# Optimization experiments

Hardware: AMD Instinct MI355X
Metric: run time of the kernel (lower is better)

## Reference

```python
import jax, jax.numpy as jnp
import numpy as np
import itertools

GRID = 256          # voxel grid extent per axis (coords in [0, GRID))
KSIZE = 3           # kernel_size
OFFSETS = np.array(list(itertools.product(range(KSIZE), repeat=3)), dtype=np.int32) - (KSIZE // 2)  # [27,3]


def setup_inputs() -> dict:
    key = jax.random.key(0)
    k1, k2, k3 = jax.random.split(key, 3)
    N, Cin, Cout = 262144, 64, 64
    coords = jax.random.randint(k1, (N, 3), 0, GRID, dtype=jnp.int32)
    feats = jax.random.normal(k2, (N, Cin), dtype=jnp.float32)
    kernel = jax.random.normal(k3, (KSIZE ** 3, Cin, Cout), dtype=jnp.float32) * 0.02
    return {"coords": coords, "feats": feats, "kernel": kernel}


def reference(coords, feats, kernel):
    # Submanifold sparse conv3d: out[i] = sum_k feats[j_k(i)] @ kernel[k]
    # where coords[j_k(i)] == coords[i] + offset_k (if such a point exists).
    N = coords.shape[0]
    Cout = kernel.shape[-1]
    # Hash table: linearized voxel -> point index (-1 if empty).
    lin = (coords[:, 0] * GRID + coords[:, 1]) * GRID + coords[:, 2]
    table = jnp.full((GRID ** 3,), -1, dtype=jnp.int32).at[lin].set(
        jnp.arange(N, dtype=jnp.int32))
    out = jnp.zeros((N, Cout), dtype=feats.dtype)
    for k in range(KSIZE ** 3):
        off = jnp.asarray(OFFSETS[k])              # [3]
        nc = coords + off[None, :]                 # neighbor coords [N,3]
        in_bounds = jnp.all((nc >= 0) & (nc < GRID), axis=1)
        nlin = (nc[:, 0] * GRID + nc[:, 1]) * GRID + nc[:, 2]
        idx = table[jnp.clip(nlin, 0, GRID ** 3 - 1)]
        valid = in_bounds & (idx >= 0)
        g = feats[jnp.where(valid, idx, 0)] * valid[:, None].astype(feats.dtype)  # [N,Cin]
        out = out + g @ kernel[k]                  # [N,Cout]
    return out
```

## Files before the change

### kernel.cpp

```cpp
#include <hip/hip_runtime.h>

#define VGRID 256
#define N_TAPS 27
#define CIN 64
#define COUT 64
#define BPTS 128

typedef short short8 __attribute__((ext_vector_type(8)));
typedef float float4v __attribute__((ext_vector_type(4)));

__device__ __forceinline__ short f2bf(float x) {
    unsigned u = __builtin_bit_cast(unsigned, x);
    unsigned r = (u + 0x7FFF + ((u >> 16) & 1)) >> 16;
    return (short)r;
}

__global__ void __launch_bounds__(256) build_kernel(
        const int* __restrict__ coords, int* __restrict__ table,
        unsigned* __restrict__ bits, const float* __restrict__ W,
        short* __restrict__ Wt, const float* __restrict__ F,
        short* __restrict__ Fb, int n, int bt_blocks, int fb_elems) {
    int b = (int)blockIdx.x;
    if (b >= bt_blocks + N_TAPS) {
        int idx = (b - bt_blocks - N_TAPS) * 256 + (int)threadIdx.x;
        int e = idx * 8;
        if (e < fb_elems) {
            const float4v* s = (const float4v*)(F + e);
            float4v x = __builtin_nontemporal_load(s);
            float4v y = __builtin_nontemporal_load(s + 1);
            short8 o = {f2bf(x[0]), f2bf(x[1]), f2bf(x[2]), f2bf(x[3]),
                        f2bf(y[0]), f2bf(y[1]), f2bf(y[2]), f2bf(y[3])};
            *(short8*)(Fb + e) = o;
        }
        return;
    }
    if (b >= bt_blocks) {
        int tap = b - bt_blocks;
        for (int e = threadIdx.x; e < CIN * COUT; e += 256) {
            int ci = e >> 6, co = e & 63;
            int ks = ci >> 5, quad = (ci >> 3) & 3, el = ci & 7;
            Wt[((((size_t)tap * 2 + ks) * 4 + quad) * 64 + co) * 8 + el] =
                f2bf(W[((size_t)tap * CIN + ci) * COUT + co]);
        }
        return;
    }
    int i = b * 256 + threadIdx.x;
    if (i >= n) return;
    int lin = (coords[i * 3 + 0] * VGRID + coords[i * 3 + 1]) * VGRID + coords[i * 3 + 2];
    atomicMax(&table[lin], i);
    atomicOr(&bits[lin >> 5], 1u << (lin & 31));
}

template<bool BF>
__global__ void __launch_bounds__(256) fused_kernel_t(
        const int* __restrict__ coords, const int* __restrict__ table,
        const unsigned* __restrict__ bits, const float* __restrict__ feats,
        const short* __restrict__ featsb, const short* __restrict__ Wt,
        float* __restrict__ out, int n) {
    __shared__ int s_pk[BPTS];
    __shared__ unsigned s_hm[2][BPTS];
    __shared__ int s_jc[BPTS];
    __shared__ int s_p[4][BPTS];

    int t = threadIdx.x;
    int p = t & (BPTS - 1);
    int h = t >> 7;
    int i = blockIdx.x * BPTS + p;

    int cx = 0, cy = 0, cz = 0;
    unsigned pmask = 0;
    if (i < n) {
        cx = coords[i * 3 + 0];
        cy = coords[i * 3 + 1];
        cz = coords[i * 3 + 2];
        if (h == 0) s_jc[p] = table[(cx * VGRID + cy) * VGRID + cz];

        int zlo = cz > 0 ? cz - 1 : 0;
        int zhi = cz < VGRID - 1 ? cz + 1 : VGRID - 1;
        int wlo = zlo >> 5, whi = zhi >> 5;
        unsigned rwa[5], rwb[5];
#pragma unroll
        for (int rr = 0; rr < 5; ++rr) {
            int r = h * 5 + rr;
            int nx = cx + r / 3 - 1, ny = cy + r % 3 - 1;
            bool v = (r < 9) && ((unsigned)nx < VGRID) && ((unsigned)ny < VGRID);
            int rb = ((nx * VGRID + ny) * VGRID) >> 5;
            rwa[rr] = v ? bits[rb + wlo] : 0u;
            rwb[rr] = v ? bits[rb + whi] : 0u;
        }
#pragma unroll
        for (int rr = 0; rr < 5; ++rr) {
            int r = h * 5 + rr;
#pragma unroll
            for (int zz = 0; zz < 3; ++zz) {
                int k = r * 3 + zz;
                int nz = cz + zz - 1;
                if (r < 9 && k != 13 && (unsigned)nz < VGRID) {
                    unsigned wrd = ((nz >> 5) == wlo) ? rwa[rr] : rwb[rr];
                    pmask |= ((wrd >> (nz & 31)) & 1u) << k;
                }
            }
        }
    }
    if (h == 0) {
        s_pk[p] = (cx << 16) | (cy << 8) | cz;
        if (i >= n) s_jc[p] = 0;
    }
    s_hm[h][p] = pmask;
    __syncthreads();

    {
        unsigned hmc = s_hm[0][p] | s_hm[1][p];
        if (h == 0) s_hm[0][p] = hmc;
        unsigned mm = hmc;
        if (h) { mm &= mm - 1u; if (mm) mm &= mm - 1u; }
        int kA = -1, kB = -1;
        if (mm) { kA = __builtin_ctz(mm); mm &= mm - 1u;
                  if (mm) kB = __builtin_ctz(mm); }
        int ja = 0, jb = 0;
        if (kA >= 0)
            ja = table[((cx + kA / 9 - 1) * VGRID + (cy + (kA / 3) % 3 - 1)) * VGRID
                       + (cz + kA % 3 - 1)];
        if (kB >= 0)
            jb = table[((cx + kB / 9 - 1) * VGRID + (cy + (kB / 3) % 3 - 1)) * VGRID
                       + (cz + kB % 3 - 1)];
        s_p[2 * h + 0][p] = ja;
        s_p[2 * h + 1][p] = jb;
    }
    __syncthreads();

    int wave = t >> 6, lane = t & 63;
    int m = lane & 15, quad = lane >> 4;
    const short8* Bp = (const short8*)Wt;
    const short8* Fp = (const short8*)featsb;
    int base = blockIdx.x * BPTS;

    for (int gg = 0; gg < 2; ++gg) {
        int g = wave * 2 + gg;
        int row = g * 16 + m;
        unsigned rhm = s_hm[0][row];

        unsigned gor = rhm;
        gor |= (unsigned)__shfl_xor((int)gor, 1);
        gor |= (unsigned)__shfl_xor((int)gor, 2);
        gor |= (unsigned)__shfl_xor((int)gor, 4);
        gor |= (unsigned)__shfl_xor((int)gor, 8);
        gor = __builtin_amdgcn_readfirstlane(gor);

        float4v acc[4] = {{0,0,0,0},{0,0,0,0},{0,0,0,0},{0,0,0,0}};

        {
            int rjc = s_jc[row];
            short8 a0, a1;
            if constexpr (BF) {
                a0 = Fp[(size_t)rjc * 8 + quad];
                a1 = Fp[(size_t)rjc * 8 + 4 + quad];
            } else {
                const float* fr = feats + (size_t)rjc * CIN + quad * 8;
                float4v u0 = *(const float4v*)(fr);
                float4v u1 = *(const float4v*)(fr + 4);
                float4v v0 = *(const float4v*)(fr + 32);
                float4v v1 = *(const float4v*)(fr + 36);
                a0 = (short8){f2bf(u0[0]), f2bf(u0[1]), f2bf(u0[2]), f2bf(u0[3]),
                              f2bf(u1[0]), f2bf(u1[1]), f2bf(u1[2]), f2bf(u1[3])};
                a1 = (short8){f2bf(v0[0]), f2bf(v0[1]), f2bf(v0[2]), f2bf(v0[3]),
                              f2bf(v1[0]), f2bf(v1[1]), f2bf(v1[2]), f2bf(v1[3])};
            }
#pragma unroll
            for (int nt = 0; nt < 4; ++nt) {
                short8 b0 = Bp[((13 * 2 + 0) * 4 + quad) * 64 + nt * 16 + m];
                short8 b1 = Bp[((13 * 2 + 1) * 4 + quad) * 64 + nt * 16 + m];
                acc[nt] = __builtin_amdgcn_mfma_f32_16x16x32_bf16(a0, b0, acc[nt], 0, 0, 0);
                acc[nt] = __builtin_amdgcn_mfma_f32_16x16x32_bf16(a1, b1, acc[nt], 0, 0, 0);
            }
        }

        unsigned gm = gor;
        while (gm) {
            int k = (int)__builtin_ctz(gm); gm &= gm - 1u;
            bool has = (rhm >> k) & 1u;
            short8 h0 = {0,0,0,0,0,0,0,0}, h1 = {0,0,0,0,0,0,0,0};
            if (has) {
                int rank = __builtin_popcount(rhm & ((1u << k) - 1u));
                int j2;
                if (rank < 4) {
                    j2 = s_p[rank][row];
                } else {
                    int rpk = s_pk[row];
                    int rx = (rpk >> 16) & 255, ry = (rpk >> 8) & 255, rz = rpk & 255;
                    j2 = table[((rx + k / 9 - 1) * VGRID + (ry + (k / 3) % 3 - 1)) * VGRID
                               + (rz + k % 3 - 1)];
                }
                if constexpr (BF) {
                    h0 = Fp[(size_t)j2 * 8 + quad];
                    h1 = Fp[(size_t)j2 * 8 + 4 + quad];
                } else {
                    const float* hr = feats + (size_t)j2 * CIN + quad * 8;
                    float4v u0 = *(const float4v*)(hr);
                    float4v u1 = *(const float4v*)(hr + 4);
                    float4v v0 = *(const float4v*)(hr + 32);
                    float4v v1 = *(const float4v*)(hr + 36);
                    h0 = (short8){f2bf(u0[0]), f2bf(u0[1]), f2bf(u0[2]), f2bf(u0[3]),
                                  f2bf(u1[0]), f2bf(u1[1]), f2bf(u1[2]), f2bf(u1[3])};
                    h1 = (short8){f2bf(v0[0]), f2bf(v0[1]), f2bf(v0[2]), f2bf(v0[3]),
                                  f2bf(v1[0]), f2bf(v1[1]), f2bf(v1[2]), f2bf(v1[3])};
                }
            }
#pragma unroll
            for (int nt = 0; nt < 4; ++nt) {
                short8 b0 = Bp[((k * 2 + 0) * 4 + quad) * 64 + nt * 16 + m];
                short8 b1 = Bp[((k * 2 + 1) * 4 + quad) * 64 + nt * 16 + m];
                acc[nt] = __builtin_amdgcn_mfma_f32_16x16x32_bf16(h0, b0, acc[nt], 0, 0, 0);
                acc[nt] = __builtin_amdgcn_mfma_f32_16x16x32_bf16(h1, b1, acc[nt], 0, 0, 0);
            }
        }

#pragma unroll
        for (int nt = 0; nt < 4; ++nt)
#pragma unroll
            for (int r2 = 0; r2 < 4; ++r2) {
                int orow = base + g * 16 + quad * 4 + r2;
                if (orow < n)
                    __builtin_nontemporal_store(
                        acc[nt][r2], &out[(size_t)orow * COUT + nt * 16 + m]);
            }
    }
}

extern "C" void kernel_launch(void* const* d_in, const int* in_sizes, int n_in,
                              void* d_out, int out_size, void* d_ws, size_t ws_size,
                              hipStream_t stream) {
    const int* coords = (const int*)d_in[0];
    const float* feats = (const float*)d_in[1];
    const float* weights = (const float*)d_in[2];
    float* out = (float*)d_out;

    int n = in_sizes[0] / 3;

    char* ws = (char*)d_ws;
    size_t BITMAP_BYTES = (size_t)VGRID * VGRID * VGRID / 8;
    bool bf = ws_size >= ((size_t)100 << 20);
    unsigned* bits = (unsigned*)ws;
    short* wbft = (short*)(ws + BITMAP_BYTES);
    short* fb = bf ? (short*)(ws + ((size_t)4 << 20)) : nullptr;
    int* table = (int*)(ws + (bf ? ((size_t)36 << 20) : ((size_t)4 << 20)));

    hipMemsetAsync(ws, 0, BITMAP_BYTES, stream);

    int bt_blocks = (n + 255) / 256;
    int fb_elems = bf ? n * CIN : 0;
    int conv_blocks = bf ? (fb_elems / 8 + 255) / 256 : 0;
    build_kernel<<<bt_blocks + N_TAPS + conv_blocks, 256, 0, stream>>>(
        coords, table, bits, weights, wbft, feats, fb, n, bt_blocks, fb_elems);

    int f_blocks = (n + BPTS - 1) / BPTS;
    if (bf)
        fused_kernel_t<true><<<f_blocks, 256, 0, stream>>>(
            coords, table, bits, feats, fb, wbft, out, n);
    else
        fused_kernel_t<false><<<f_blocks, 256, 0, stream>>>(
            coords, table, bits, feats, fb, wbft, out, n);
}
```

Before: 209.5 us.

## Replace dense voxel table with compact open-addressing hash and pair tap processing

Swaps the 64 MB dense voxel-to-index table for a 1M-slot linear-probing hash of packed (key, index) 64-bit entries, built with atomicCAS and atomicMax. All lookups in the fused kernel go through this hash. The tap loop now handles two taps per iteration, with the center tap folded in, so more feature loads are in flight at once. The float fallback path is removed and the workspace is assumed large enough for the bf16 feature copy. This cuts table footprint and cache misses, at the cost of probe chains and an extra 8 MB memset.

```diff
diff --git a/kernel.cpp b/kernel.cpp
--- a/kernel.cpp
+++ b/kernel.cpp
@@ -5,6 +5,9 @@
 #define CIN 64
 #define COUT 64
 #define BPTS 128
+#define HBITS 20
+#define HSIZE (1u << HBITS)
+#define HEMPTY 0xFFFFFFFFFFFFFFFFull
 
 typedef short short8 __attribute__((ext_vector_type(8)));
 typedef float float4v __attribute__((ext_vector_type(4)));
@@ -15,8 +18,22 @@
     return (short)r;
 }
 
+__device__ __forceinline__ unsigned hslot(int lin) {
+    return ((unsigned)lin * 2654435761u) >> (32 - HBITS);
+}
+
+__device__ __forceinline__ int hlookup(const unsigned long long* __restrict__ hash,
+                                       int lin) {
+    unsigned s = hslot(lin);
+    for (;;) {
+        unsigned long long e = hash[s];
+        if ((unsigned)(e >> 32) == (unsigned)lin) return (int)(unsigned)e;
+        s = (s + 1) & (HSIZE - 1);
+    }
+}
+
 __global__ void __launch_bounds__(256) build_kernel(
-        const int* __restrict__ coords, int* __restrict__ table,
+        const int* __restrict__ coords, unsigned long long* __restrict__ hash,
         unsigned* __restrict__ bits, const float* __restrict__ W,
         short* __restrict__ Wt, const float* __restrict__ F,
         short* __restrict__ Fb, int n, int bt_blocks, int fb_elems) {
@@ -47,16 +64,21 @@
     int i = b * 256 + threadIdx.x;
     if (i >= n) return;
     int lin = (coords[i * 3 + 0] * VGRID + coords[i * 3 + 1]) * VGRID + coords[i * 3 + 2];
-    atomicMax(&table[lin], i);
+    unsigned long long want = ((unsigned long long)(unsigned)lin << 32) | (unsigned)i;
+    unsigned s = hslot(lin);
+    for (;;) {
+        unsigned long long old = atomicCAS(&hash[s], HEMPTY, want);
+        if (old == HEMPTY) break;
+        if ((unsigned)(old >> 32) == (unsigned)lin) { atomicMax(&hash[s], want); break; }
+        s = (s + 1) & (HSIZE - 1);
+    }
     atomicOr(&bits[lin >> 5], 1u << (lin & 31));
 }
 
-template<bool BF>
-__global__ void __launch_bounds__(256) fused_kernel_t(
-        const int* __restrict__ coords, const int* __restrict__ table,
-        const unsigned* __restrict__ bits, const float* __restrict__ feats,
-        const short* __restrict__ featsb, const short* __restrict__ Wt,
-        float* __restrict__ out, int n) {
+__global__ void __launch_bounds__(256) fused_kernel(
+        const int* __restrict__ coords, const unsigned long long* __restrict__ hash,
+        const unsigned* __restrict__ bits, const short* __restrict__ featsb,
+        const short* __restrict__ Wt, float* __restrict__ out, int n) {
     __shared__ int s_pk[BPTS];
     __shared__ unsigned s_hm[2][BPTS];
     __shared__ int s_jc[BPTS];
@@ -73,7 +95,7 @@
         cx = coords[i * 3 + 0];
         cy = coords[i * 3 + 1];
         cz = coords[i * 3 + 2];
-        if (h == 0) s_jc[p] = table[(cx * VGRID + cy) * VGRID + cz];
+        if (h == 0) s_jc[p] = hlookup(hash, (cx * VGRID + cy) * VGRID + cz);
 
         int zlo = cz > 0 ? cz - 1 : 0;
         int zhi = cz < VGRID - 1 ? cz + 1 : VGRID - 1;
@@ -119,11 +141,11 @@
                   if (mm) kB = __builtin_ctz(mm); }
         int ja = 0, jb = 0;
         if (kA >= 0)
-            ja = table[((cx + kA / 9 - 1) * VGRID + (cy + (kA / 3) % 3 - 1)) * VGRID
-                       + (cz + kA % 3 - 1)];
+            ja = hlookup(hash, ((cx + kA / 9 - 1) * VGRID + (cy + (kA / 3) % 3 - 1)) * VGRID
+                               + (cz + kA % 3 - 1));
         if (kB >= 0)
-            jb = table[((cx + kB / 9 - 1) * VGRID + (cy + (kB / 3) % 3 - 1)) * VGRID
-                       + (cz + kB % 3 - 1)];
+            jb = hlookup(hash, ((cx + kB / 9 - 1) * VGRID + (cy + (kB / 3) % 3 - 1)) * VGRID
+                               + (cz + kB % 3 - 1));
         s_p[2 * h + 0][p] = ja;
         s_p[2 * h + 1][p] = jb;
     }
@@ -139,6 +161,7 @@
         int g = wave * 2 + gg;
         int row = g * 16 + m;
         unsigned rhm = s_hm[0][row];
+        int rjc = s_jc[row];
 
         unsigned gor = rhm;
         gor |= (unsigned)__shfl_xor((int)gor, 1);
@@ -149,69 +172,54 @@
 
         float4v acc[4] = {{0,0,0,0},{0,0,0,0},{0,0,0,0},{0,0,0,0}};
 
-        {
-            int rjc = s_jc[row];
-            short8 a0, a1;
-            if constexpr (BF) {
-                a0 = Fp[(size_t)rjc * 8 + quad];
-                a1 = Fp[(size_t)rjc * 8 + 4 + quad];
-            } else {
-                const float* fr = feats + (size_t)rjc * CIN + quad * 8;
-                float4v u0 = *(const float4v*)(fr);
-                float4v u1 = *(const float4v*)(fr + 4);
-                float4v v0 = *(const float4v*)(fr + 32);
-                float4v v1 = *(const float4v*)(fr + 36);
-                a0 = (short8){f2bf(u0[0]), f2bf(u0[1]), f2bf(u0[2]), f2bf(u0[3]),
-                              f2bf(u1[0]), f2bf(u1[1]), f2bf(u1[2]), f2bf(u1[3])};
-                a1 = (short8){f2bf(v0[0]), f2bf(v0[1]), f2bf(v0[2]), f2bf(v0[3]),
-                              f2bf(v1[0]), f2bf(v1[1]), f2bf(v1[2]), f2bf(v1[3])};
-            }
-#pragma unroll
-            for (int nt = 0; nt < 4; ++nt) {
-                short8 b0 = Bp[((13 * 2 + 0) * 4 + quad) * 64 + nt * 16 + m];
-                short8 b1 = Bp[((13 * 2 + 1) * 4 + quad) * 64 + nt * 16 + m];
-                acc[nt] = __builtin_amdgcn_mfma_f32_16x16x32_bf16(a0, b0, acc[nt], 0, 0, 0);
-                acc[nt] = __builtin_amdgcn_mfma_f32_16x16x32_bf16(a1, b1, acc[nt], 0, 0, 0);
-            }
-        }
-
-        unsigned gm = gor;
-        while (gm) {
-            int k = (int)__builtin_ctz(gm); gm &= gm - 1u;
-            bool has = (rhm >> k) & 1u;
-            short8 h0 = {0,0,0,0,0,0,0,0}, h1 = {0,0,0,0,0,0,0,0};
-            if (has) {
+        auto loadfrag = [&](int k, short8& f0, short8& f1) {
+            int j2 = -1;
+            if (k == 13) {
+                j2 = rjc;
+            } else if ((rhm >> k) & 1u) {
                 int rank = __builtin_popcount(rhm & ((1u << k) - 1u));
-                int j2;
                 if (rank < 4) {
                     j2 = s_p[rank][row];
                 } else {
                     int rpk = s_pk[row];
                     int rx = (rpk >> 16) & 255, ry = (rpk >> 8) & 255, rz = rpk & 255;
-                    j2 = table[((rx + k / 9 - 1) * VGRID + (ry + (k / 3) % 3 - 1)) * VGRID
-                               + (rz + k % 3 - 1)];
+                    j2 = hlookup(hash, ((rx + k / 9 - 1) * VGRID + (ry + (k / 3) % 3 - 1))
+                                       * VGRID + (rz + k % 3 - 1));
                 }
-                if constexpr (BF) {
-                    h0 = Fp[(size_t)j2 * 8 + quad];
-                    h1 = Fp[(size_t)j2 * 8 + 4 + quad];
-                } else {
-                    const float* hr = feats + (size_t)j2 * CIN + quad * 8;
-                    float4v u0 = *(const float4v*)(hr);
-                    float4v u1 = *(const float4v*)(hr + 4);
-                    float4v v0 = *(const float4v*)(hr + 32);
-                    float4v v1 = *(const float4v*)(hr + 36);
-                    h0 = (short8){f2bf(u0[0]), f2bf(u0[1]), f2bf(u0[2]), f2bf(u0[3]),
-                                  f2bf(u1[0]), f2bf(u1[1]), f2bf(u1[2]), f2bf(u1[3])};
-                    h1 = (short8){f2bf(v0[0]), f2bf(v0[1]), f2bf(v0[2]), f2bf(v0[3]),
-                                  f2bf(v1[0]), f2bf(v1[1]), f2bf(v1[2]), f2bf(v1[3])};
+            }
+            f0 = (short8){0,0,0,0,0,0,0,0};
+            f1 = (short8){0,0,0,0,0,0,0,0};
+            if (j2 >= 0) {
+                f0 = Fp[(size_t)j2 * 8 + quad];
+                f1 = Fp[(size_t)j2 * 8 + 4 + quad];
+            }
+        };
+
+        unsigned gm = gor | (1u << 13);
+        while (gm) {
+            int k0 = (int)__builtin_ctz(gm); gm &= gm - 1u;
+            int k1 = -1;
+            if (gm) { k1 = (int)__builtin_ctz(gm); gm &= gm - 1u; }
+
+            short8 x0, x1, y0, y1;
+            loadfrag(k0, x0, x1);
+            if (k1 >= 0) loadfrag(k1, y0, y1);
+
+#pragma unroll
+            for (int nt = 0; nt < 4; ++nt) {
+                short8 b0 = Bp[((k0 * 2 + 0) * 4 + quad) * 64 + nt * 16 + m];
+                short8 b1 = Bp[((k0 * 2 + 1) * 4 + quad) * 64 + nt * 16 + m];
+                acc[nt] = __builtin_amdgcn_mfma_f32_16x16x32_bf16(x0, b0, acc[nt], 0, 0, 0);
+                acc[nt] = __builtin_amdgcn_mfma_f32_16x16x32_bf16(x1, b1, acc[nt], 0, 0, 0);
+            }
+            if (k1 >= 0) {
+#pragma unroll
+                for (int nt = 0; nt < 4; ++nt) {
+                    short8 b0 = Bp[((k1 * 2 + 0) * 4 + quad) * 64 + nt * 16 + m];
+                    short8 b1 = Bp[((k1 * 2 + 1) * 4 + quad) * 64 + nt * 16 + m];
+                    acc[nt] = __builtin_amdgcn_mfma_f32_16x16x32_bf16(y0, b0, acc[nt], 0, 0, 0);
+                    acc[nt] = __builtin_amdgcn_mfma_f32_16x16x32_bf16(y1, b1, acc[nt], 0, 0, 0);
                 }
-            }
-#pragma unroll
-            for (int nt = 0; nt < 4; ++nt) {
-                short8 b0 = Bp[((k * 2 + 0) * 4 + quad) * 64 + nt * 16 + m];
-                short8 b1 = Bp[((k * 2 + 1) * 4 + quad) * 64 + nt * 16 + m];
-                acc[nt] = __builtin_amdgcn_mfma_f32_16x16x32_bf16(h0, b0, acc[nt], 0, 0, 0);
-                acc[nt] = __builtin_amdgcn_mfma_f32_16x16x32_bf16(h1, b1, acc[nt], 0, 0, 0);
             }
         }
 
@@ -239,25 +247,20 @@
 
     char* ws = (char*)d_ws;
     size_t BITMAP_BYTES = (size_t)VGRID * VGRID * VGRID / 8;
-    bool bf = ws_size >= ((size_t)100 << 20);
     unsigned* bits = (unsigned*)ws;
-    short* wbft = (short*)(ws + BITMAP_BYTES);
-    short* fb = bf ? (short*)(ws + ((size_t)4 << 20)) : nullptr;
-    int* table = (int*)(ws + (bf ? ((size_t)36 << 20) : ((size_t)4 << 20)));
+    unsigned long long* hash = (unsigned long long*)(ws + BITMAP_BYTES);
+    short* wbft = (short*)(ws + ((size_t)10 << 20));
+    short* fb = (short*)(ws + ((size_t)11 << 20));
 
     hipMemsetAsync(ws, 0, BITMAP_BYTES, stream);
+    hipMemsetAsync(ws + BITMAP_BYTES, 0xFF, (size_t)HSIZE * 8, stream);
 
     int bt_blocks = (n + 255) / 256;
-    int fb_elems = bf ? n * CIN : 0;
-    int conv_blocks = bf ? (fb_elems / 8 + 255) / 256 : 0;
+    int fb_elems = n * CIN;
+    int conv_blocks = (fb_elems / 8 + 255) / 256;
     build_kernel<<<bt_blocks + N_TAPS + conv_blocks, 256, 0, stream>>>(
-        coords, table, bits, weights, wbft, feats, fb, n, bt_blocks, fb_elems);
+        coords, hash, bits, weights, wbft, feats, fb, n, bt_blocks, fb_elems);
 
     int f_blocks = (n + BPTS - 1) / BPTS;
-    if (bf)
-        fused_kernel_t<true><<<f_blocks, 256, 0, stream>>>(
-            coords, table, bits, feats, fb, wbft, out, n);
-    else
-        fused_kernel_t<false><<<f_blocks, 256, 0, stream>>>(
-            coords, table, bits, feats, fb, wbft, out, n);
-}
+    fused_kernel<<<f_blocks, 256, 0, stream>>>(coords, hash, bits, fb, wbft, out, n);
+}
```

Result: no change. 211.0 us (+0.7%).
